# Kernel tuning notes

Hardware: AMD Instinct MI355X
Metric: run time of the kernel (lower is better)

Reference implementation:

```python
import jax, jax.numpy as jnp
import numpy as np

H, W = 300, 400            # grid_size
RES = 0.1                  # resolution (m/pixel)
X0, X1 = -20.0, 20.0       # x_range
Y0, Y1 = -10.0, 30.0       # y_range
Z0, Z1 = -3.0, 4.0         # z_range
MAX_INT = 255.0            # max_intensity
N_MAX = 128.0              # density_normalize
K_SAMPLES = 512            # >= max Bresenham steps inside grid (diag <= 400)


def _rasterize_polyline(pts_xy):
    """DDA line rasterization of an ego-frame polyline -> [H, W] binary grid.
    Matches the Bresenham + 3x3 stamp (width 2 or 3 -> half_w=1) of the original."""
    px = jnp.trunc((pts_xy[:, 0] - X0) / RES)  # int() truncation as in original
    py = jnp.trunc((pts_xy[:, 1] - Y0) / RES)
    p = jnp.stack([px, py], axis=-1)           # [N, 2] pixel coords (float)
    a, b = p[:-1], p[1:]                        # segment endpoints [S, 2]

    def inb(q):
        return (q[:, 0] >= 0) & (q[:, 0] < W) & (q[:, 1] >= 0) & (q[:, 1] < H)

    valid = inb(a) | inb(b)                     # draw if either endpoint in bounds
    lo = jnp.array([0.0, 0.0], jnp.float32)
    hi = jnp.array([W - 1.0, H - 1.0], jnp.float32)
    a = jnp.clip(a, lo, hi)
    b = jnp.clip(b, lo, hi)

    dmax = jnp.max(jnp.abs(b - a), axis=-1)     # [S] major-axis length in pixels
    k = jnp.arange(K_SAMPLES, dtype=jnp.float32)
    t = jnp.minimum(k[None, :], dmax[:, None]) / jnp.maximum(dmax[:, None], 1.0)
    pts = a[:, None, :] + t[..., None] * (b - a)[:, None, :]   # [S, K, 2]
    pix = jnp.round(pts).astype(jnp.int32)

    offs = jnp.arange(-1, 2)                    # half_w = width//2 = 1 -> 3x3 stamp
    xs = pix[..., 0][..., None, None] + offs[:, None]          # [S, K, 3, 1]
    ys = pix[..., 1][..., None, None] + offs[None, :]          # [S, K, 1, 3]
    xs, ys = jnp.broadcast_arrays(xs, ys)
    val = jnp.broadcast_to(valid.astype(jnp.float32)[:, None, None, None], xs.shape)
    # out-of-bounds stamped pixels are dropped, as in the original bounds check
    return jnp.zeros((H, W), jnp.float32).at[ys, xs].max(val, mode="drop")


def _rasterize_lidar(points):
    """[N,4] (x,y,z,intensity) -> [3,H,W] (height, mean intensity, log density)."""
    x, y, z, inten = points[:, 0], points[:, 1], points[:, 2], points[:, 3]
    mask = (x >= X0) & (x < X1) & (y >= Y0) & (y < Y1)
    px = jnp.clip(((x - X0) / RES).astype(jnp.int32), 0, W - 1)
    py = jnp.clip(((y - Y0) / RES).astype(jnp.int32), 0, H - 1)
    w = mask.astype(jnp.float32)
    neg_inf = jnp.float32(-jnp.inf)

    hmax = jnp.full((H, W), neg_inf, jnp.float32).at[py, px].max(
        jnp.where(mask, z, neg_inf))
    hmax = jnp.where(jnp.isneginf(hmax), 0.0, hmax)  # empty cells -> 0 BEFORE norm

    isum = jnp.zeros((H, W), jnp.float32).at[py, px].add(inten * w)
    cnt = jnp.zeros((H, W), jnp.float32).at[py, px].add(w)
    imean = jnp.where(cnt > 0, isum / jnp.maximum(cnt, 1.0), 0.0)

    h = jnp.clip((hmax - Z0) / (Z1 - Z0), 0.0, 1.0)
    i = jnp.clip(imean / MAX_INT, 0.0, 1.0)
    d = jnp.clip(jnp.log1p(cnt) / jnp.log(1.0 + N_MAX), 0.0, 1.0)
    return jnp.stack([h, i, d])


def setup_inputs() -> dict:
    key = jax.random.key(0)
    k1, k2 = jax.random.split(key)
    # LiDAR: 4M points, slightly wider than the ROI so ~some get filtered
    u = jax.random.uniform(k1, (4_000_000, 4), dtype=jnp.float32)
    lo = jnp.array([-25.0, -15.0, -3.0, 0.0], jnp.float32)
    hi = jnp.array([25.0, 35.0, 4.0, 255.0], jnp.float32)
    lidar_points = lo + u * (hi - lo)
    # trajectory: smooth forward path in ego frame
    ty = jnp.linspace(0.0, 25.0, 50, dtype=jnp.float32)
    tx = 2.0 * jnp.sin(0.3 * ty)
    trajectory = jnp.stack([tx, ty], axis=-1)
    # OSM polyline: random walk in world frame (ego at origin)
    steps = 0.5 * jax.random.normal(k2, (2000, 2), dtype=jnp.float32)
    osm_coords = jnp.cumsum(steps, axis=0) + jnp.array([0.0, 10.0], jnp.float32)
    ego_pose = jnp.zeros((3,), jnp.float32)
    return {"lidar_points": lidar_points, "trajectory": trajectory,
            "osm_coords": osm_coords, "ego_pose": ego_pose}


def reference(lidar_points, trajectory, osm_coords, ego_pose):
    lidar_bev = _rasterize_lidar(lidar_points)                 # [3,H,W]
    traj_bev = _rasterize_polyline(trajectory)[None]           # [1,H,W]
    # world -> ego for OSM coords
    cy, sy = jnp.cos(-ego_pose[2]), jnp.sin(-ego_pose[2])
    d = osm_coords - ego_pose[:2]
    osm_ego = jnp.stack([d[:, 0] * cy - d[:, 1] * sy,
                         d[:, 0] * sy + d[:, 1] * cy], axis=-1)
    map_bev = _rasterize_polyline(osm_ego)[None]               # [1,H,W]
    return jnp.concatenate([lidar_bev, traj_bev, map_bev], axis=0)  # [5,H,W]
```

## Files before the change

### kernel.cpp

```cpp
#include <hip/hip_runtime.h>
#include <math.h>

#define GH 300
#define GW 400
#define GHW (GH * GW)

#define TCOLS 25
#define TROWS 19
#define T_TILES (TCOLS * TROWS)
#define B1 1024
#define Q 16
#define CAP2 8192

#define SMEM_BYTES 45152

__device__ __forceinline__ bool bin_point(float x, float y, int& px, int& py) {
    if (!(x >= -20.0f && x < 20.0f && y >= -10.0f && y < 30.0f)) return false;
    float qx = __fmul_rn(__fsub_rn(x, -20.0f), 10.0f);
    float qy = __fmul_rn(__fsub_rn(y, -10.0f), 10.0f);
    px = min(max((int)qx, 0), GW - 1);
    py = min(max((int)qy, 0), GH - 1);
    return true;
}

__device__ __forceinline__ void tile_prefix_wave0(const unsigned* src, unsigned* dst) {
    int lane = threadIdx.x;
    if (lane < 64) {
        unsigned run = 0;
        for (int c = 0; c < T_TILES; c += 64) {
            int idx = c + lane;
            unsigned v = (idx < T_TILES) ? src[idx] : 0u;
            unsigned orig = v;
#pragma unroll
            for (int d = 1; d < 64; d <<= 1) {
                unsigned u = __shfl_up(v, d, 64);
                if (lane >= d) v += u;
            }
            if (idx < T_TILES) dst[idx] = run + (v - orig);
            run += __shfl(v, 63, 64);
        }
        if (lane == 0) dst[T_TILES] = run;
    }
}

__device__ __forceinline__ unsigned block_scan_excl_1024(unsigned c, unsigned* wsum, int l) {
    int lane = l & 63, wid = l >> 6;
    unsigned v = c;
#pragma unroll
    for (int d = 1; d < 64; d <<= 1) {
        unsigned u = __shfl_up(v, d, 64);
        if (lane >= d) v += u;
    }
    if (lane == 63) wsum[wid] = v;
    __syncthreads();
    if (l < 16) {
        unsigned wv = wsum[l], worig = wv;
#pragma unroll
        for (int d = 1; d < 16; d <<= 1) {
            unsigned u = __shfl_up(wv, d, 16);
            if (l >= d) wv += u;
        }
        wsum[l] = wv - worig;
    }
    __syncthreads();
    return (v - c) + wsum[wid];
}

__device__ __forceinline__ bool make_record(float4 p, unsigned& rec, int& tile) {
    int px, py;
    if (!bin_point(p.x, p.y, px, py)) return false;
    tile = (py >> 4) * TCOLS + (px >> 4);
    int local = ((py & 15) << 4) | (px & 15);
    int z16 = min(max((int)rintf(__fmul_rn(__fadd_rn(p.z, 3.0f), 65535.0f / 7.0f)), 0), 65535);
    int i8 = min(max((int)rintf(p.w), 0), 255);
    rec = ((unsigned)z16 << 16) | ((unsigned)i8 << 8) | (unsigned)local;
    return true;
}

__global__ __launch_bounds__(256) void p1_kernel(const float4* __restrict__ pts, int n,
                                                 int per_block,
                                                 unsigned* __restrict__ staged,
                                                 unsigned* __restrict__ pref_t,
                                                 float* __restrict__ out) {
    __shared__ unsigned lbuf[256 * Q];
    __shared__ unsigned short ltile[256 * Q];
    __shared__ unsigned cnt[T_TILES];
    __shared__ unsigned pref[T_TILES + 1];
    __shared__ unsigned cur[T_TILES];
    for (int t = threadIdx.x; t < T_TILES; t += 256) cnt[t] = 0;
    float4* z4 = (float4*)(out + 3 * GHW);
    for (int j = blockIdx.x * 256 + (int)threadIdx.x; j < (2 * GHW) / 4; j += B1 * 256)
        z4[j] = make_float4(0.0f, 0.0f, 0.0f, 0.0f);
    __syncthreads();

    int start = blockIdx.x * per_block;
    int end = min(start + per_block, n);
    int nmine = 0;
    int i = start + (int)threadIdx.x;
    for (; i + 7 * 256 < end; i += 8 * 256) {
        float4 p[8];
#pragma unroll
        for (int j = 0; j < 8; ++j) p[j] = pts[i + j * 256];
#pragma unroll
        for (int j = 0; j < 8; ++j) {
            unsigned r;
            int tile;
            if (make_record(p[j], r, tile)) {
                lbuf[nmine * 256 + threadIdx.x] = r;
                ltile[nmine * 256 + threadIdx.x] = (unsigned short)tile;
                ++nmine;
                atomicAdd(&cnt[tile], 1u);
            }
        }
    }
    for (; i < end; i += 256) {
        unsigned r;
        int tile;
        if (make_record(pts[i], r, tile)) {
            lbuf[nmine * 256 + threadIdx.x] = r;
            ltile[nmine * 256 + threadIdx.x] = (unsigned short)tile;
            ++nmine;
            atomicAdd(&cnt[tile], 1u);
        }
    }
    __syncthreads();
    tile_prefix_wave0(cnt, pref);
    __syncthreads();
    for (int t = threadIdx.x; t < T_TILES; t += 256) cur[t] = pref[t];
    for (int t = threadIdx.x; t <= T_TILES; t += 256)
        pref_t[t * B1 + blockIdx.x] = pref[t];
    __syncthreads();
    size_t base = (size_t)blockIdx.x * (size_t)per_block;
    for (int j = 0; j < nmine; ++j) {
        unsigned r = lbuf[j * 256 + threadIdx.x];
        int tile = (int)ltile[j * 256 + threadIdx.x];
        unsigned pos = atomicAdd(&cur[tile], 1u);
        staged[base + pos] = r;
    }
}

__device__ void do_poly_segment(int seg, const float2* __restrict__ traj, int ntraj,
                                const float2* __restrict__ osm, int nosm,
                                const float* __restrict__ ego, float* __restrict__ out) {
    int ntseg = ntraj - 1;
    int noseg = nosm - 1;
    if (seg >= ntseg + noseg) return;
    const float2* pts;
    float* out_ch;
    bool use_ego;
    if (seg < ntseg) {
        pts = traj + seg;
        out_ch = out + 3 * GHW;
        use_ego = false;
    } else {
        pts = osm + (seg - ntseg);
        out_ch = out + 4 * GHW;
        use_ego = true;
    }
    float2 P0 = pts[0];
    float2 P1 = pts[1];
    if (use_ego) {
        float yaw = ego[2];
        float cy = cosf(-yaw), sy = sinf(-yaw);
        float ex = ego[0], ey = ego[1];
        float d0x = __fsub_rn(P0.x, ex), d0y = __fsub_rn(P0.y, ey);
        float d1x = __fsub_rn(P1.x, ex), d1y = __fsub_rn(P1.y, ey);
        P0.x = __fsub_rn(__fmul_rn(d0x, cy), __fmul_rn(d0y, sy));
        P0.y = __fadd_rn(__fmul_rn(d0x, sy), __fmul_rn(d0y, cy));
        P1.x = __fsub_rn(__fmul_rn(d1x, cy), __fmul_rn(d1y, sy));
        P1.y = __fadd_rn(__fmul_rn(d1x, sy), __fmul_rn(d1y, cy));
    }
    double ax = trunc(__ddiv_rn(__dadd_rn((double)P0.x, 20.0), 0.1));
    double ay = trunc(__ddiv_rn(__dadd_rn((double)P0.y, 10.0), 0.1));
    double bx = trunc(__ddiv_rn(__dadd_rn((double)P1.x, 20.0), 0.1));
    double by = trunc(__ddiv_rn(__dadd_rn((double)P1.y, 10.0), 0.1));
    bool inA = (ax >= 0.0) && (ax < (double)GW) && (ay >= 0.0) && (ay < (double)GH);
    bool inB = (bx >= 0.0) && (bx < (double)GW) && (by >= 0.0) && (by < (double)GH);
    if (!(inA || inB)) return;
    ax = fmin(fmax(ax, 0.0), (double)(GW - 1));
    ay = fmin(fmax(ay, 0.0), (double)(GH - 1));
    bx = fmin(fmax(bx, 0.0), (double)(GW - 1));
    by = fmin(fmax(by, 0.0), (double)(GH - 1));
    double dx = __dsub_rn(bx, ax);
    double dy = __dsub_rn(by, ay);
    double dmax = fmax(fabs(dx), fabs(dy));
    double denom = fmax(dmax, 1.0);
    int kmax = (int)dmax;
    for (int k = 0; k <= kmax; ++k) {
        double t = __ddiv_rn(fmin((double)k, dmax), denom);
        double ptx = __dadd_rn(ax, __dmul_rn(t, dx));
        double pty = __dadd_rn(ay, __dmul_rn(t, dy));
        int cx = (int)rint(ptx);
        int cc = (int)rint(pty);
#pragma unroll
        for (int oy = -1; oy <= 1; ++oy) {
#pragma unroll
            for (int ox = -1; ox <= 1; ++ox) {
                int xx = cx + ox;
                int yy = cc + oy;
                if (xx < 0) xx += GW;
                if (yy < 0) yy += GH;
                if (xx >= 0 && xx < GW && yy >= 0 && yy < GH) {
                    out_ch[yy * GW + xx] = 1.0f;
                }
            }
        }
    }
}

__global__ __launch_bounds__(1024) void p2_kernel(const unsigned* __restrict__ staged,
                                                  const unsigned* __restrict__ pref_t,
                                                  int per_block,
                                                  float* __restrict__ out,
                                                  const float2* __restrict__ traj, int ntraj,
                                                  const float2* __restrict__ osm, int nosm,
                                                  const float* __restrict__ ego) {
    __shared__ char smem[SMEM_BYTES];
    int l = threadIdx.x;

    if (blockIdx.x >= T_TILES) {
        double* ax_s = (double*)(smem);
        double* ay_s = (double*)(smem + 8192);
        double* dx_s = (double*)(smem + 16384);
        double* dy_s = (double*)(smem + 24576);
        unsigned* cum = (unsigned*)(smem + 32768);
        unsigned* chan = (unsigned*)(smem + 36868);
        unsigned* wsum = (unsigned*)(smem + 40964);

        int pb = blockIdx.x - T_TILES;
        int seg = pb * 1024 + l;
        int ntseg = ntraj - 1;
        int noseg = nosm - 1;
        int nseg = ntseg + noseg;
        unsigned jobs = 0;
        if (seg < nseg) {
            const float2* pts;
            bool use_ego;
            unsigned ch;
            if (seg < ntseg) {
                pts = traj + seg;
                ch = 3u;
                use_ego = false;
            } else {
                pts = osm + (seg - ntseg);
                ch = 4u;
                use_ego = true;
            }
            float2 P0 = pts[0];
            float2 P1 = pts[1];
            if (use_ego) {
                float yaw = ego[2];
                float cy = cosf(-yaw), sy = sinf(-yaw);
                float ex = ego[0], ey = ego[1];
                float d0x = __fsub_rn(P0.x, ex), d0y = __fsub_rn(P0.y, ey);
                float d1x = __fsub_rn(P1.x, ex), d1y = __fsub_rn(P1.y, ey);
                P0.x = __fsub_rn(__fmul_rn(d0x, cy), __fmul_rn(d0y, sy));
                P0.y = __fadd_rn(__fmul_rn(d0x, sy), __fmul_rn(d0y, cy));
                P1.x = __fsub_rn(__fmul_rn(d1x, cy), __fmul_rn(d1y, sy));
                P1.y = __fadd_rn(__fmul_rn(d1x, sy), __fmul_rn(d1y, cy));
            }
            double ax = trunc(__ddiv_rn(__dadd_rn((double)P0.x, 20.0), 0.1));
            double ay = trunc(__ddiv_rn(__dadd_rn((double)P0.y, 10.0), 0.1));
            double bx = trunc(__ddiv_rn(__dadd_rn((double)P1.x, 20.0), 0.1));
            double by = trunc(__ddiv_rn(__dadd_rn((double)P1.y, 10.0), 0.1));
            bool inA = (ax >= 0.0) && (ax < (double)GW) && (ay >= 0.0) && (ay < (double)GH);
            bool inB = (bx >= 0.0) && (bx < (double)GW) && (by >= 0.0) && (by < (double)GH);
            if (inA || inB) {
                ax = fmin(fmax(ax, 0.0), (double)(GW - 1));
                ay = fmin(fmax(ay, 0.0), (double)(GH - 1));
                bx = fmin(fmax(bx, 0.0), (double)(GW - 1));
                by = fmin(fmax(by, 0.0), (double)(GH - 1));
                double dx = __dsub_rn(bx, ax);
                double dy = __dsub_rn(by, ay);
                double dmax = fmax(fabs(dx), fabs(dy));
                jobs = (unsigned)((int)dmax) + 1u;
                ax_s[l] = ax;
                ay_s[l] = ay;
                dx_s[l] = dx;
                dy_s[l] = dy;
                chan[l] = ch;
            }
        }
        unsigned excl = block_scan_excl_1024(jobs, wsum, l);
        cum[l] = excl;
        if (l == 1023) cum[1024] = excl + jobs;
        __syncthreads();
        unsigned tot = cum[1024];
        for (unsigned j = l; j < tot; j += 1024) {
            unsigned lo = 0, hi = 1024;
#pragma unroll
            for (int it = 0; it < 10; ++it) {
                unsigned mid = (lo + hi) >> 1;
                if (cum[mid] <= j) lo = mid; else hi = mid;
            }
            int k = (int)(j - cum[lo]);
            double ax = ax_s[lo], ay = ay_s[lo], dx = dx_s[lo], dy = dy_s[lo];
            double dmax = fmax(fabs(dx), fabs(dy));
            double denom = fmax(dmax, 1.0);
            double t = __ddiv_rn(fmin((double)k, dmax), denom);
            double ptx = __dadd_rn(ax, __dmul_rn(t, dx));
            double pty = __dadd_rn(ay, __dmul_rn(t, dy));
            int cx = (int)rint(ptx);
            int cc = (int)rint(pty);
            float* out_ch = out + (size_t)chan[lo] * GHW;
#pragma unroll
            for (int oy = -1; oy <= 1; ++oy) {
#pragma unroll
                for (int ox = -1; ox <= 1; ++ox) {
                    int xx = cx + ox;
                    int yy = cc + oy;
                    if (xx < 0) xx += GW;
                    if (yy < 0) yy += GH;
                    if (xx >= 0 && xx < GW && yy >= 0 && yy < GH) {
                        out_ch[yy * GW + xx] = 1.0f;
                    }
                }
            }
        }
        return;
    }

    unsigned* addr_lds = (unsigned*)(smem);
    unsigned* cumB = (unsigned*)(smem + 32768);
    unsigned* wsum = (unsigned*)(smem + 36868);
    unsigned* ic4 = (unsigned*)(smem + 36932);
    unsigned* zmax4 = (unsigned*)(smem + 41028);
    if (l < 1024) {
        ic4[l] = 0;
        zmax4[l] = 0;
    }

    int bid = blockIdx.x;
    const int NX = 8;
    const int q = T_TILES / NX;
    const int r = T_TILES % NX;
    int xk = bid % NX;
    int jj = bid / NX;
    int t = (xk < r ? xk * (q + 1) : r * (q + 1) + (xk - r) * q) + jj;

    unsigned a0 = pref_t[t * B1 + l];
    unsigned a1 = pref_t[(t + 1) * B1 + l];
    unsigned c = a1 - a0;
    unsigned myBase = block_scan_excl_1024(c, wsum, l);
    cumB[l] = myBase;
    if (l == B1 - 1) cumB[B1] = myBase + c;
    __syncthreads();
    unsigned nrec = cumB[B1];
    unsigned myAddr0 = (unsigned)l * (unsigned)per_block + a0;
    unsigned* icR = ic4 + ((l >> 6) & 3) * 256;
    unsigned* zmR = zmax4 + ((l >> 6) & 3) * 256;

    for (unsigned b0 = 0; b0 < nrec; b0 += CAP2) {
        unsigned bh = min(b0 + CAP2, nrec);
        unsigned j0 = max(myBase, b0);
        unsigned j1 = min(myBase + c, bh);
        for (unsigned j = j0; j < j1; ++j)
            addr_lds[j - b0] = myAddr0 + (j - myBase);
        __syncthreads();
        unsigned nb = bh - b0;
        unsigned ad[8], rr[8];
        bool val[8];
#pragma unroll
        for (int i2 = 0; i2 < 8; ++i2) {
            unsigned ki = (unsigned)l + (unsigned)(i2 * 1024);
            val[i2] = ki < nb;
            ad[i2] = val[i2] ? addr_lds[ki] : 0u;
        }
#pragma unroll
        for (int i2 = 0; i2 < 8; ++i2) {
            if (val[i2]) rr[i2] = staged[ad[i2]];
        }
#pragma unroll
        for (int i2 = 0; i2 < 8; ++i2) {
            if (val[i2]) {
                unsigned r2 = rr[i2];
                int local = (int)(r2 & 255u);
                atomicMax(&zmR[local], r2 >> 16);
                atomicAdd(&icR[local], (1u << 20) | ((r2 >> 8) & 255u));
            }
        }
        __syncthreads();
    }

    if (l < 256) {
        unsigned v2 = ic4[l] + ic4[256 + l] + ic4[512 + l] + ic4[768 + l];
        unsigned zfin = max(max(zmax4[l], zmax4[256 + l]),
                            max(zmax4[512 + l], zmax4[768 + l]));
        int trow = t / TCOLS, tcol = t % TCOLS;
        int gy = trow * 16 + (l >> 4);
        int gx = tcol * 16 + (l & 15);
        if (gy < GH) {
            const float inv7 = 1.0f / 7.0f;
            const float invlog129 = 1.0f / 4.8598124043616719e+00f;
            float h, ich, dd;
            if (v2 == 0) {
                h = fminf(fmaxf(__fmul_rn(3.0f, inv7), 0.0f), 1.0f);
                ich = 0.0f;
                dd = 0.0f;
            } else {
                unsigned cnt = v2 >> 20;
                float sum8 = (float)(v2 & 0xFFFFFu);
                h = fminf((float)zfin * (1.0f / 65535.0f), 1.0f);
                ich = fminf(__fdiv_rn(sum8, __fmul_rn((float)cnt, 255.0f)), 1.0f);
                dd = fminf(__fmul_rn(log1pf((float)cnt), invlog129), 1.0f);
            }
            int idx = gy * GW + gx;
            out[0 * GHW + idx] = h;
            out[1 * GHW + idx] = ich;
            out[2 * GHW + idx] = dd;
        }
    }
}

__global__ __launch_bounds__(256) void polylines_kernel(const float2* __restrict__ traj,
                                                        int ntraj,
                                                        const float2* __restrict__ osm, int nosm,
                                                        const float* __restrict__ ego,
                                                        float* __restrict__ out) {
    int seg = blockIdx.x * 256 + (int)threadIdx.x;
    do_poly_segment(seg, traj, ntraj, osm, nosm, ego, out);
}

__global__ __launch_bounds__(256) void init_kernel(float* __restrict__ out) {
    int i = blockIdx.x * blockDim.x + threadIdx.x;
    if (i < GHW) {
        out[0 * GHW + i] = -INFINITY;
        out[1 * GHW + i] = 0.0f;
        out[2 * GHW + i] = 0.0f;
        out[3 * GHW + i] = 0.0f;
        out[4 * GHW + i] = 0.0f;
    }
}

__device__ __forceinline__ void atomicMaxFloat(float* addr, float val) {
    if (val >= 0.0f) {
        atomicMax((int*)addr, __float_as_int(val));
    } else {
        atomicMin((unsigned int*)addr, (unsigned int)__float_as_int(val));
    }
}

__global__ __launch_bounds__(256) void lidar_kernel(const float4* __restrict__ pts, int n,
                                                    float* __restrict__ out) {
    int i = blockIdx.x * blockDim.x + threadIdx.x;
    if (i >= n) return;
    float4 p = pts[i];
    int px, py;
    if (!bin_point(p.x, p.y, px, py)) return;
    int idx = py * GW + px;
    atomicMaxFloat(&out[0 * GHW + idx], p.z);
    atomicAdd(&out[1 * GHW + idx], p.w);
    atomicAdd(&out[2 * GHW + idx], 1.0f);
}

__global__ __launch_bounds__(256) void finalize_kernel(float* __restrict__ out) {
    int i = blockIdx.x * blockDim.x + threadIdx.x;
    if (i >= GHW) return;
    float hm = out[0 * GHW + i];
    float isum = out[1 * GHW + i];
    float c = out[2 * GHW + i];
    if (hm == -INFINITY) hm = 0.0f;
    const float inv7 = 1.0f / 7.0f;
    const float inv255 = 1.0f / 255.0f;
    const float invlog129 = 1.0f / 4.8598124043616719e+00f;
    float h = fminf(fmaxf(__fmul_rn(__fadd_rn(hm, 3.0f), inv7), 0.0f), 1.0f);
    float im = (c > 0.0f) ? __fdiv_rn(isum, fmaxf(c, 1.0f)) : 0.0f;
    float ich = fminf(fmaxf(__fmul_rn(im, inv255), 0.0f), 1.0f);
    float dd = fminf(fmaxf(__fmul_rn(log1pf(c), invlog129), 0.0f), 1.0f);
    out[0 * GHW + i] = h;
    out[1 * GHW + i] = ich;
    out[2 * GHW + i] = dd;
}

extern "C" void kernel_launch(void* const* d_in, const int* in_sizes, int n_in,
                              void* d_out, int out_size, void* d_ws, size_t ws_size,
                              hipStream_t stream) {
    const float* lidar = (const float*)d_in[0];
    const float* traj = (const float*)d_in[1];
    const float* osm = (const float*)d_in[2];
    const float* ego = (const float*)d_in[3];
    float* out = (float*)d_out;

    int n_lidar = in_sizes[0] / 4;
    int n_traj = in_sizes[1] / 2;
    int n_osm = in_sizes[2] / 2;
    int nseg = (n_traj - 1) + (n_osm - 1);
    int npb = (nseg + 1023) / 1024;

    int per_block = (n_lidar + B1 - 1) / B1;
    size_t staged_bytes = (size_t)B1 * (size_t)per_block * 4;
    size_t pref_bytes = (size_t)(T_TILES + 1) * B1 * 4;
    size_t need = staged_bytes + pref_bytes;

    if (ws_size >= need && per_block <= 256 * Q) {
        char* w = (char*)d_ws;
        unsigned* staged = (unsigned*)w;
        unsigned* pref_t = (unsigned*)(w + staged_bytes);

        p1_kernel<<<B1, 256, 0, stream>>>((const float4*)lidar, n_lidar, per_block, staged,
                                          pref_t, out);
        p2_kernel<<<T_TILES + npb, 1024, 0, stream>>>(staged, pref_t, per_block, out,
                                                      (const float2*)traj, n_traj,
                                                      (const float2*)osm, n_osm, ego);
    } else {
        init_kernel<<<(GHW + 255) / 256, 256, 0, stream>>>(out);
        lidar_kernel<<<(n_lidar + 255) / 256, 256, 0, stream>>>((const float4*)lidar, n_lidar,
                                                                out);
        finalize_kernel<<<(GHW + 255) / 256, 256, 0, stream>>>(out);
        polylines_kernel<<<(nseg + 255) / 256, 256, 0, stream>>>((const float2*)traj, n_traj,
                                                                 (const float2*)osm, n_osm, ego,
                                                                 out);
    }
}
```

Before: 128.5 us.

## Gather staged records as 16-byte groups with lane masks instead of single words

The per-tile accumulation pass now indexes staged records in aligned groups of four. Each entry in the LDS address list encodes the group index plus a 4-bit validity mask, and the pass loads a uint4 per entry and applies atomics only for the masked lanes. The goal is fewer, wider global loads and a smaller address buffer in LDS, with the shared-memory footprint reduced to match. The cost is wasted lanes where runs are partially aligned and extra mask logic. A 4-wide remainder loop is also added to the binning pass.

```diff
diff --git a/kernel.cpp b/kernel.cpp
--- a/kernel.cpp
+++ b/kernel.cpp
@@ -10,9 +10,9 @@
 #define T_TILES (TCOLS * TROWS)
 #define B1 1024
 #define Q 16
-#define CAP2 8192
-
-#define SMEM_BYTES 45152
+#define CAPG 4096
+
+#define SMEM_BYTES 41056
 
 __device__ __forceinline__ bool bin_point(float x, float y, int& px, int& py) {
     if (!(x >= -20.0f && x < 20.0f && y >= -10.0f && y < 30.0f)) return false;
@@ -103,6 +103,22 @@
         for (int j = 0; j < 8; ++j) p[j] = pts[i + j * 256];
 #pragma unroll
         for (int j = 0; j < 8; ++j) {
+            unsigned r;
+            int tile;
+            if (make_record(p[j], r, tile)) {
+                lbuf[nmine * 256 + threadIdx.x] = r;
+                ltile[nmine * 256 + threadIdx.x] = (unsigned short)tile;
+                ++nmine;
+                atomicAdd(&cnt[tile], 1u);
+            }
+        }
+    }
+    for (; i + 3 * 256 < end; i += 4 * 256) {
+        float4 p[4];
+#pragma unroll
+        for (int j = 0; j < 4; ++j) p[j] = pts[i + j * 256];
+#pragma unroll
+        for (int j = 0; j < 4; ++j) {
             unsigned r;
             int tile;
             if (make_record(p[j], r, tile)) {
@@ -321,14 +337,12 @@
     }
 
     unsigned* addr_lds = (unsigned*)(smem);
-    unsigned* cumB = (unsigned*)(smem + 32768);
-    unsigned* wsum = (unsigned*)(smem + 36868);
-    unsigned* ic4 = (unsigned*)(smem + 36932);
-    unsigned* zmax4 = (unsigned*)(smem + 41028);
-    if (l < 1024) {
-        ic4[l] = 0;
-        zmax4[l] = 0;
-    }
+    unsigned* cumB = (unsigned*)(smem + 16384);
+    unsigned* wsum = (unsigned*)(smem + 20484);
+    unsigned* ic4 = (unsigned*)(smem + 20548);
+    unsigned* zmax4 = (unsigned*)(smem + 24644);
+    ic4[l] = 0;
+    zmax4[l] = 0;
 
     int bid = blockIdx.x;
     const int NX = 8;
@@ -341,42 +355,58 @@
     unsigned a0 = pref_t[t * B1 + l];
     unsigned a1 = pref_t[(t + 1) * B1 + l];
     unsigned c = a1 - a0;
-    unsigned myBase = block_scan_excl_1024(c, wsum, l);
-    cumB[l] = myBase;
-    if (l == B1 - 1) cumB[B1] = myBase + c;
-    __syncthreads();
-    unsigned nrec = cumB[B1];
     unsigned myAddr0 = (unsigned)l * (unsigned)per_block + a0;
+    unsigned g0 = myAddr0 >> 2;
+    unsigned ng = c ? (((myAddr0 + c + 3u) >> 2) - g0) : 0u;
+    unsigned myGBase = block_scan_excl_1024(ng, wsum, l);
+    cumB[l] = myGBase;
+    if (l == B1 - 1) cumB[B1] = myGBase + ng;
+    __syncthreads();
+    unsigned ntot = cumB[B1];
     unsigned* icR = ic4 + ((l >> 6) & 3) * 256;
     unsigned* zmR = zmax4 + ((l >> 6) & 3) * 256;
-
-    for (unsigned b0 = 0; b0 < nrec; b0 += CAP2) {
-        unsigned bh = min(b0 + CAP2, nrec);
-        unsigned j0 = max(myBase, b0);
-        unsigned j1 = min(myBase + c, bh);
-        for (unsigned j = j0; j < j1; ++j)
-            addr_lds[j - b0] = myAddr0 + (j - myBase);
+    unsigned s_abs = myAddr0, e_abs = myAddr0 + c;
+
+    for (unsigned b0 = 0; b0 < ntot; b0 += CAPG) {
+        unsigned bh = min(b0 + CAPG, ntot);
+        unsigned j0 = max(myGBase, b0);
+        unsigned j1 = min(myGBase + ng, bh);
+        for (unsigned j = j0; j < j1; ++j) {
+            unsigned g = g0 + (j - myGBase);
+            unsigned glo = g << 2;
+            unsigned lo = s_abs > glo ? s_abs - glo : 0u;
+            unsigned hi = (e_abs < glo + 4u) ? e_abs - glo : 4u;
+            unsigned mask = ((1u << hi) - 1u) & ~((1u << lo) - 1u);
+            addr_lds[j - b0] = (g << 4) | mask;
+        }
         __syncthreads();
         unsigned nb = bh - b0;
-        unsigned ad[8], rr[8];
-        bool val[8];
-#pragma unroll
-        for (int i2 = 0; i2 < 8; ++i2) {
+        unsigned desc[4];
+        uint4 gv[4];
+        bool val[4];
+#pragma unroll
+        for (int i2 = 0; i2 < 4; ++i2) {
             unsigned ki = (unsigned)l + (unsigned)(i2 * 1024);
             val[i2] = ki < nb;
-            ad[i2] = val[i2] ? addr_lds[ki] : 0u;
-        }
-#pragma unroll
-        for (int i2 = 0; i2 < 8; ++i2) {
-            if (val[i2]) rr[i2] = staged[ad[i2]];
-        }
-#pragma unroll
-        for (int i2 = 0; i2 < 8; ++i2) {
+            desc[i2] = val[i2] ? addr_lds[ki] : 0u;
+        }
+#pragma unroll
+        for (int i2 = 0; i2 < 4; ++i2) {
+            if (val[i2]) gv[i2] = ((const uint4*)staged)[desc[i2] >> 4];
+        }
+#pragma unroll
+        for (int i2 = 0; i2 < 4; ++i2) {
             if (val[i2]) {
-                unsigned r2 = rr[i2];
-                int local = (int)(r2 & 255u);
-                atomicMax(&zmR[local], r2 >> 16);
-                atomicAdd(&icR[local], (1u << 20) | ((r2 >> 8) & 255u));
+                unsigned m = desc[i2] & 15u;
+#pragma unroll
+                for (int jb = 0; jb < 4; ++jb) {
+                    if (m & (1u << jb)) {
+                        unsigned r2 = ((const unsigned*)&gv[i2])[jb];
+                        int local = (int)(r2 & 255u);
+                        atomicMax(&zmR[local], r2 >> 16);
+                        atomicAdd(&icR[local], (1u << 20) | ((r2 >> 8) & 255u));
+                    }
+                }
             }
         }
         __syncthreads();
```

After: 131.6 us. 1.02x slower.
